# Performance work log

Measured on AMD Instinct MI355X. Metric: run time of the kernel, lower is better.

## Reference

```python
import jax, jax.numpy as jnp
import numpy as np


def setup_inputs() -> dict:
    key = jax.random.key(0)
    k1, k2, k3, k4 = jax.random.split(key, 4)
    b, l, v, s = 2, 2048, 8, 64
    return {
        "query": jax.random.normal(k1, (b, l, v, s), dtype=jnp.float32),
        "key": jax.random.normal(k2, (b, l, v, s), dtype=jnp.float32),
        "value": jax.random.normal(k3, (b, l, v, s), dtype=jnp.float32),
        "label_arr": jax.random.randint(k4, (b, l), 0, 8, dtype=jnp.int64),
    }


def reference(query, key, value, label_arr):
    # query/key/value: (b, l, v, s); label_arr computed into a mask in the
    # original code but never applied, so it does not affect the math.
    b, l, v, s = query.shape
    scale = 1.0 / np.sqrt(s).astype(np.float32)
    # key summed over the v (head) axis -> pooled key per token: (b, l, s)
    sum_tot_vec = key.sum(axis=2)
    # scores[b,l,v,m] = <query[b,l,v,:], sum_tot_vec[b,m,:]>  (the torch per-v loop, batched)
    scores = jnp.einsum("blvs,bms->blvm", query, sum_tot_vec)
    A = jax.nn.softmax(scale * scores, axis=-1)  # (b, l, v, l)
    # V[b,l,v,s] = sum_m A[b,l,v,m] * value[b,m,v,s]  (the broadcast-multiply+sum, as a matmul)
    V = jnp.einsum("blvm,bmvs->blvs", A, value)
    return V
```

## Files before the change

kernel.cpp:

```cpp
#include <hip/hip_runtime.h>


#define BB 2
#define LL 2048
#define HH 8
#define DD 64

typedef __attribute__((ext_vector_type(8)))  short  short8;
typedef __attribute__((ext_vector_type(16))) float  float16v;

static __device__ inline unsigned short f2bf(float x) {
    union { float f; unsigned u; } v; v.f = x;
    unsigned r = v.u + 0x7FFF + ((v.u >> 16) & 1);
    return (unsigned short)(r >> 16);
}
static __device__ inline unsigned pk_bf2(float x, float y) {
    return (unsigned)f2bf(x) | ((unsigned)f2bf(y) << 16);
}

__global__ void pool_kernel(const float* __restrict__ key,
                            unsigned short* __restrict__ kswz) {
    int c  = blockIdx.x * blockDim.x + threadIdx.x;
    int r  = c >> 3;
    int ck = c & 7;
    int ks = ck >> 1, hf = ck & 1;
    int b = r >> 11, ml = r & 2047;
    int T = ml >> 5, ln = ml & 31;

    const float* base = key + ((size_t)r * HH) * DD + ks * 16 + hf * 8;
    float s[8];
#pragma unroll
    for (int j = 0; j < 8; ++j) s[j] = 0.f;
#pragma unroll
    for (int v = 0; v < HH; ++v) {
        float4 f0 = *(const float4*)(base + v * DD);
        float4 f1 = *(const float4*)(base + v * DD + 4);
        s[0] += f0.x; s[1] += f0.y; s[2] += f0.z; s[3] += f0.w;
        s[4] += f1.x; s[5] += f1.y; s[6] += f1.z; s[7] += f1.w;
    }
    union { short8 v; unsigned u[4]; } o;
#pragma unroll
    for (int i = 0; i < 4; ++i) o.u[i] = pk_bf2(s[2 * i], s[2 * i + 1]);
    *(short8*)(kswz + ((((size_t)b * 64 + T) * 4 + ks) * 512)
                    + (hf * 32 + ln) * 8) = o.v;
}

__global__ void vswz_kernel(const float* __restrict__ value,
                            unsigned short* __restrict__ vswz, int bh0) {
    int blk = blockIdx.x;
    int mt  = blk & 31;
    int bhl = blk >> 5;
    int bh  = bh0 + bhl;
    int h = bh & 7, b = bh >> 3;
    int m0 = mt * 64;
    int tid = threadIdx.x;

    __shared__ __align__(16) float Vl[64][68];

#pragma unroll
    for (int k = 0; k < 4; ++k) {
        int f = tid + k * 256;
        int r = f >> 4;
        int cc = (f & 15) * 4;
        float4 t = *(const float4*)(value +
            (((size_t)(b * LL + m0 + r)) * HH + h) * DD + cc);
        *(float4*)&Vl[r][cc] = t;
    }
    __syncthreads();

#pragma unroll
    for (int k = 0; k < 2; ++k) {
        int c    = tid + k * 256;
        int Tl   = c >> 8;
        int t    = (c >> 7) & 1;
        int vh   = (c >> 6) & 1;
        int lane = c & 63;
        int ln = lane & 31, half = lane >> 5;
        union { short8 v; unsigned short u[8]; } o;
#pragma unroll
        for (int jj = 0; jj < 8; ++jj) {
            int r2  = t * 8 + jj;
            int key = (r2 & 3) + 8 * (r2 >> 2) + 4 * half;
            o.u[jj] = f2bf(Vl[Tl * 32 + key][vh * 32 + ln]);
        }
        *(short8*)(vswz + ((((size_t)bhl * 64 + (mt * 2 + Tl)) * 4 + t * 2 + vh) * 512)
                        + lane * 8) = o.v;
    }
}

__global__ __launch_bounds__(512, 4)
void attn_kernel(const float* __restrict__ query,
                 const unsigned short* __restrict__ kswz,
                 const unsigned short* __restrict__ vswz,
                 float* __restrict__ out, int bh0) {
    constexpr int NIT = 8;

    int bid = blockIdx.x;
    int qt  = bid & 63;
    int bhl = bid >> 6;
    int bh  = bh0 + bhl;
    int h = bh & 7, b = bh >> 3;

    int tid  = threadIdx.x;
    int lane = tid & 63;
    int wv   = tid >> 6;
    int ln   = lane & 31;
    int half = lane >> 5;

    __shared__ float O4[4][32][DD];
    __shared__ float lsumL[4][64];
    __shared__ float invL[32];

    short8 qf[4];
    const float* qbase = query + (((size_t)(b * LL + qt * 32 + ln)) * HH + h) * DD;
#pragma unroll
    for (int ks = 0; ks < 4; ++ks) {
        const float4* qp = (const float4*)(qbase + ks * 16 + half * 8);
        float4 t0 = qp[0], t1 = qp[1];
        union { short8 v; unsigned u[4]; } uq;
        uq.u[0] = pk_bf2(t0.x * 0.125f, t0.y * 0.125f);
        uq.u[1] = pk_bf2(t0.z * 0.125f, t0.w * 0.125f);
        uq.u[2] = pk_bf2(t1.x * 0.125f, t1.y * 0.125f);
        uq.u[3] = pk_bf2(t1.z * 0.125f, t1.w * 0.125f);
        qf[ks] = uq.v;
    }

    const unsigned short* kp0 = kswz + (((size_t)b * 64 + wv * 8) * 4) * 512
                                     + (size_t)lane * 8;
    const unsigned short* vp0 = vswz + (((size_t)bhl * 64 + wv * 8) * 4) * 512
                                     + (size_t)lane * 8;

    float16v o0, o1;
#pragma unroll
    for (int i = 0; i < 16; ++i) { o0[i] = 0.f; o1[i] = 0.f; }
    float lsum = 0.f;

    short8 kf[4];
#pragma unroll
    for (int ks = 0; ks < 4; ++ks) kf[ks] = *(const short8*)(kp0 + ks * 512);

#pragma unroll
    for (int it = 0; it < NIT; ++it) {
        short8 vf[4];
#pragma unroll
        for (int u = 0; u < 4; ++u)
            vf[u] = *(const short8*)(vp0 + it * 2048 + u * 512);

        float16v sacc;
#pragma unroll
        for (int i = 0; i < 16; ++i) sacc[i] = 0.f;
#pragma unroll
        for (int ks = 0; ks < 4; ++ks)
            sacc = __builtin_amdgcn_mfma_f32_32x32x16_bf16(kf[ks], qf[ks], sacc, 0, 0, 0);

        short8 kn[4];
        if (it + 1 < NIT) {
#pragma unroll
            for (int ks = 0; ks < 4; ++ks)
                kn[ks] = *(const short8*)(kp0 + (it + 1) * 2048 + ks * 512);
        }

        union { short8 v[2]; unsigned u[8]; } pu;
#pragma unroll
        for (int i = 0; i < 8; ++i) {
            union { float f; unsigned u; } e0, e1;
            e0.f = __expf(sacc[2 * i]);
            e1.f = __expf(sacc[2 * i + 1]);
            lsum += e0.f + e1.f;
            pu.u[i] = __builtin_amdgcn_perm(e1.u + 0x8000u, e0.u + 0x8000u, 0x07060302u);
        }

#pragma unroll
        for (int t = 0; t < 2; ++t) {
            o0 = __builtin_amdgcn_mfma_f32_32x32x16_bf16(pu.v[t], vf[t * 2 + 0], o0, 0, 0, 0);
            o1 = __builtin_amdgcn_mfma_f32_32x32x16_bf16(pu.v[t], vf[t * 2 + 1], o1, 0, 0, 0);
        }

        if (it + 1 < NIT) {
#pragma unroll
            for (int ks = 0; ks < 4; ++ks) kf[ks] = kn[ks];
        }
    }

    if (wv < 4) {
        lsumL[wv][lane] = lsum;
#pragma unroll
        for (int r = 0; r < 16; ++r) {
            int row = (r & 3) + 8 * (r >> 2) + 4 * half;
            O4[wv][row][ln]      = o0[r];
            O4[wv][row][32 + ln] = o1[r];
        }
    }
    __syncthreads();
    if (wv >= 4) {
        lsumL[wv - 4][lane] += lsum;
#pragma unroll
        for (int r = 0; r < 16; ++r) {
            int row = (r & 3) + 8 * (r >> 2) + 4 * half;
            O4[wv - 4][row][ln]      += o0[r];
            O4[wv - 4][row][32 + ln] += o1[r];
        }
    }
    __syncthreads();

    if (tid < 32) {
        float s = 0.f;
#pragma unroll
        for (int w = 0; w < 4; ++w) s += lsumL[w][tid] + lsumL[w][tid + 32];
        invL[tid] = 1.0f / s;
    }
    __syncthreads();

    int qrow = tid >> 4;
    int c4   = (tid & 15) * 4;
    float inv = invL[qrow];
    float4 r;
    r.x = (O4[0][qrow][c4 + 0] + O4[1][qrow][c4 + 0] + O4[2][qrow][c4 + 0] + O4[3][qrow][c4 + 0]) * inv;
    r.y = (O4[0][qrow][c4 + 1] + O4[1][qrow][c4 + 1] + O4[2][qrow][c4 + 1] + O4[3][qrow][c4 + 1]) * inv;
    r.z = (O4[0][qrow][c4 + 2] + O4[1][qrow][c4 + 2] + O4[2][qrow][c4 + 2] + O4[3][qrow][c4 + 2]) * inv;
    r.w = (O4[0][qrow][c4 + 3] + O4[1][qrow][c4 + 3] + O4[2][qrow][c4 + 3] + O4[3][qrow][c4 + 3]) * inv;
    *(float4*)(out + (((size_t)(b * LL + qt * 32 + qrow)) * HH + h) * DD + c4) = r;
}

extern "C" void kernel_launch(void* const* d_in, const int* in_sizes, int n_in,
                              void* d_out, int out_size, void* d_ws, size_t ws_size,
                              hipStream_t stream) {
    const float* query = (const float*)d_in[0];
    const float* key   = (const float*)d_in[1];
    const float* value = (const float*)d_in[2];
    float* out = (float*)d_out;

    unsigned short* kswz = (unsigned short*)d_ws;
    unsigned short* vswz = (unsigned short*)((char*)d_ws + 512 * 1024);

    size_t avail = (ws_size > (size_t)(512 * 1024)) ? ws_size - 512 * 1024 : 0;
    int nbh = (int)(avail / ((size_t)DD * LL * 2));
    if (nbh >= 16) nbh = 16; else if (nbh >= 8) nbh = 8;
    else if (nbh >= 4) nbh = 4; else if (nbh >= 2) nbh = 2; else nbh = 1;

    pool_kernel<<<(BB * LL * 8) / 256, 256, 0, stream>>>(key, kswz);

    for (int bh0 = 0; bh0 < BB * HH; bh0 += nbh) {
        vswz_kernel<<<nbh * 32, 256, 0, stream>>>(value, vswz, bh0);
        attn_kernel<<<nbh * 64, 512, 0, stream>>>(query, kswz, vswz, out, bh0);
    }
}
```

Before: 105.4 us.

## Fuse prep kernels, process 64 queries per block, use exp2 with pre-scaled keys

Merges the key pooling and value swizzle into one prep kernel and drops the workspace-size-dependent per-head loop, so only two launches remain. The attention block now covers 64 query rows with 4 waves instead of 32 rows with 8 waves, so each K/V fragment load is reused for two query groups. It also folds log2(e) into the pooled keys so the softmax can use exp2f. The trade-off is fewer blocks (512 of 256 threads) and more registers per wave, and the code now assumes the workspace can hold all 16 heads of swizzled V at once.

Result: no change. 107.2 us (+1.8%).

```diff
diff --git a/kernel.cpp b/kernel.cpp
--- a/kernel.cpp
+++ b/kernel.cpp
@@ -18,87 +18,82 @@
     return (unsigned)f2bf(x) | ((unsigned)f2bf(y) << 16);
 }
 
-__global__ void pool_kernel(const float* __restrict__ key,
-                            unsigned short* __restrict__ kswz) {
-    int c  = blockIdx.x * blockDim.x + threadIdx.x;
-    int r  = c >> 3;
-    int ck = c & 7;
-    int ks = ck >> 1, hf = ck & 1;
-    int b = r >> 11, ml = r & 2047;
-    int T = ml >> 5, ln = ml & 31;
-
-    const float* base = key + ((size_t)r * HH) * DD + ks * 16 + hf * 8;
-    float s[8];
-#pragma unroll
-    for (int j = 0; j < 8; ++j) s[j] = 0.f;
-#pragma unroll
-    for (int v = 0; v < HH; ++v) {
-        float4 f0 = *(const float4*)(base + v * DD);
-        float4 f1 = *(const float4*)(base + v * DD + 4);
-        s[0] += f0.x; s[1] += f0.y; s[2] += f0.z; s[3] += f0.w;
-        s[4] += f1.x; s[5] += f1.y; s[6] += f1.z; s[7] += f1.w;
-    }
-    union { short8 v; unsigned u[4]; } o;
-#pragma unroll
-    for (int i = 0; i < 4; ++i) o.u[i] = pk_bf2(s[2 * i], s[2 * i + 1]);
-    *(short8*)(kswz + ((((size_t)b * 64 + T) * 4 + ks) * 512)
-                    + (hf * 32 + ln) * 8) = o.v;
-}
-
-__global__ void vswz_kernel(const float* __restrict__ value,
-                            unsigned short* __restrict__ vswz, int bh0) {
-    int blk = blockIdx.x;
-    int mt  = blk & 31;
-    int bhl = blk >> 5;
-    int bh  = bh0 + bhl;
-    int h = bh & 7, b = bh >> 3;
-    int m0 = mt * 64;
+__global__ __launch_bounds__(256)
+void prep_kernel(const float* __restrict__ key, const float* __restrict__ value,
+                 unsigned short* __restrict__ kswz,
+                 unsigned short* __restrict__ vswz) {
+    __shared__ __align__(16) float Vl[64][68];
+    int bid = blockIdx.x;
     int tid = threadIdx.x;
 
-    __shared__ __align__(16) float Vl[64][68];
-
-#pragma unroll
-    for (int k = 0; k < 4; ++k) {
-        int f = tid + k * 256;
-        int r = f >> 4;
-        int cc = (f & 15) * 4;
-        float4 t = *(const float4*)(value +
-            (((size_t)(b * LL + m0 + r)) * HH + h) * DD + cc);
-        *(float4*)&Vl[r][cc] = t;
-    }
-    __syncthreads();
-
-#pragma unroll
-    for (int k = 0; k < 2; ++k) {
-        int c    = tid + k * 256;
-        int Tl   = c >> 8;
-        int t    = (c >> 7) & 1;
-        int vh   = (c >> 6) & 1;
-        int lane = c & 63;
-        int ln = lane & 31, half = lane >> 5;
-        union { short8 v; unsigned short u[8]; } o;
-#pragma unroll
-        for (int jj = 0; jj < 8; ++jj) {
-            int r2  = t * 8 + jj;
-            int key = (r2 & 3) + 8 * (r2 >> 2) + 4 * half;
-            o.u[jj] = f2bf(Vl[Tl * 32 + key][vh * 32 + ln]);
-        }
-        *(short8*)(vswz + ((((size_t)bhl * 64 + (mt * 2 + Tl)) * 4 + t * 2 + vh) * 512)
-                        + lane * 8) = o.v;
-    }
-}
-
-__global__ __launch_bounds__(512, 4)
+    if (bid < 512) {
+        int mt = bid & 31, bh = bid >> 5;
+        int h = bh & 7, b = bh >> 3;
+        int m0 = mt * 64;
+#pragma unroll
+        for (int k = 0; k < 4; ++k) {
+            int f = tid + k * 256;
+            int r = f >> 4;
+            int cc = (f & 15) * 4;
+            float4 t = *(const float4*)(value +
+                (((size_t)(b * LL + m0 + r)) * HH + h) * DD + cc);
+            *(float4*)&Vl[r][cc] = t;
+        }
+        __syncthreads();
+#pragma unroll
+        for (int k = 0; k < 2; ++k) {
+            int c    = tid + k * 256;
+            int Tl   = c >> 8;
+            int t    = (c >> 7) & 1;
+            int vh   = (c >> 6) & 1;
+            int lane = c & 63;
+            int ln = lane & 31, half = lane >> 5;
+            union { short8 v; unsigned short u[8]; } o;
+#pragma unroll
+            for (int jj = 0; jj < 8; ++jj) {
+                int r2 = t * 8 + jj;
+                int m  = (r2 & 3) + 8 * (r2 >> 2) + 4 * half;
+                o.u[jj] = f2bf(Vl[Tl * 32 + m][vh * 32 + ln]);
+            }
+            *(short8*)(vswz +
+                ((((size_t)bh * 64 + (mt * 2 + Tl)) * 4 + t * 2 + vh) * 512)
+                + lane * 8) = o.v;
+        }
+    } else {
+        const float LOG2E = 1.4426950408889634f;
+        int pb    = bid - 512;
+        int chunk = pb * 4 + (tid >> 6);
+        int lane  = tid & 63;
+        int b = chunk >> 8, T = (chunk >> 2) & 63, ks = chunk & 3;
+        int ln = lane & 31, hf = lane >> 5;
+        const float* base = key + (((size_t)(b * LL + T * 32 + ln)) * HH) * DD
+                                + ks * 16 + hf * 8;
+        float s[8];
+#pragma unroll
+        for (int j = 0; j < 8; ++j) s[j] = 0.f;
+#pragma unroll
+        for (int v = 0; v < HH; ++v) {
+            float4 f0 = *(const float4*)(base + v * DD);
+            float4 f1 = *(const float4*)(base + v * DD + 4);
+            s[0] += f0.x; s[1] += f0.y; s[2] += f0.z; s[3] += f0.w;
+            s[4] += f1.x; s[5] += f1.y; s[6] += f1.z; s[7] += f1.w;
+        }
+        union { short8 v; unsigned u[4]; } o;
+#pragma unroll
+        for (int i = 0; i < 4; ++i)
+            o.u[i] = pk_bf2(s[2 * i] * LOG2E, s[2 * i + 1] * LOG2E);
+        *(short8*)(kswz + (size_t)chunk * 512 + lane * 8) = o.v;
+    }
+}
+
+__global__ __launch_bounds__(256, 3)
 void attn_kernel(const float* __restrict__ query,
                  const unsigned short* __restrict__ kswz,
                  const unsigned short* __restrict__ vswz,
-                 float* __restrict__ out, int bh0) {
-    constexpr int NIT = 8;
-
+                 float* __restrict__ out) {
     int bid = blockIdx.x;
-    int qt  = bid & 63;
-    int bhl = bid >> 6;
-    int bh  = bh0 + bhl;
+    int bh  = bid & 15;
+    int qt  = bid >> 4;
     int h = bh & 7, b = bh >> 3;
 
     int tid  = threadIdx.x;
@@ -107,119 +102,129 @@
     int ln   = lane & 31;
     int half = lane >> 5;
 
-    __shared__ float O4[4][32][DD];
-    __shared__ float lsumL[4][64];
-    __shared__ float invL[32];
-
-    short8 qf[4];
-    const float* qbase = query + (((size_t)(b * LL + qt * 32 + ln)) * HH + h) * DD;
-#pragma unroll
-    for (int ks = 0; ks < 4; ++ks) {
-        const float4* qp = (const float4*)(qbase + ks * 16 + half * 8);
-        float4 t0 = qp[0], t1 = qp[1];
-        union { short8 v; unsigned u[4]; } uq;
-        uq.u[0] = pk_bf2(t0.x * 0.125f, t0.y * 0.125f);
-        uq.u[1] = pk_bf2(t0.z * 0.125f, t0.w * 0.125f);
-        uq.u[2] = pk_bf2(t1.x * 0.125f, t1.y * 0.125f);
-        uq.u[3] = pk_bf2(t1.z * 0.125f, t1.w * 0.125f);
-        qf[ks] = uq.v;
-    }
-
-    const unsigned short* kp0 = kswz + (((size_t)b * 64 + wv * 8) * 4) * 512
+    __shared__ float O2[2][64][68];
+    __shared__ float lsumL[4][128];
+    __shared__ float invL[64];
+
+    short8 qf[2][4];
+#pragma unroll
+    for (int g = 0; g < 2; ++g) {
+        const float* qbase = query +
+            (((size_t)(b * LL + qt * 64 + g * 32 + ln)) * HH + h) * DD;
+#pragma unroll
+        for (int ks = 0; ks < 4; ++ks) {
+            const float4* qp = (const float4*)(qbase + ks * 16 + half * 8);
+            float4 t0 = qp[0], t1 = qp[1];
+            union { short8 v; unsigned u[4]; } uq;
+            uq.u[0] = pk_bf2(t0.x * 0.125f, t0.y * 0.125f);
+            uq.u[1] = pk_bf2(t0.z * 0.125f, t0.w * 0.125f);
+            uq.u[2] = pk_bf2(t1.x * 0.125f, t1.y * 0.125f);
+            uq.u[3] = pk_bf2(t1.z * 0.125f, t1.w * 0.125f);
+            qf[g][ks] = uq.v;
+        }
+    }
+
+    const unsigned short* kp0 = kswz + (((size_t)b * 64 + wv * 16) * 4) * 512
                                      + (size_t)lane * 8;
-    const unsigned short* vp0 = vswz + (((size_t)bhl * 64 + wv * 8) * 4) * 512
+    const unsigned short* vp0 = vswz + (((size_t)bh * 64 + wv * 16) * 4) * 512
                                      + (size_t)lane * 8;
 
-    float16v o0, o1;
-#pragma unroll
-    for (int i = 0; i < 16; ++i) { o0[i] = 0.f; o1[i] = 0.f; }
-    float lsum = 0.f;
-
-    short8 kf[4];
-#pragma unroll
-    for (int ks = 0; ks < 4; ++ks) kf[ks] = *(const short8*)(kp0 + ks * 512);
-
-#pragma unroll
-    for (int it = 0; it < NIT; ++it) {
-        short8 vf[4];
+    float16v o00, o01, o10, o11;
+#pragma unroll
+    for (int i = 0; i < 16; ++i) { o00[i] = 0.f; o01[i] = 0.f; o10[i] = 0.f; o11[i] = 0.f; }
+    float ls0a = 0.f, ls0b = 0.f, ls1a = 0.f, ls1b = 0.f;
+
+#pragma unroll
+    for (int it = 0; it < 16; ++it) {
+        short8 kf[4], vf[4];
+#pragma unroll
+        for (int ks = 0; ks < 4; ++ks)
+            kf[ks] = *(const short8*)(kp0 + it * 2048 + ks * 512);
 #pragma unroll
         for (int u = 0; u < 4; ++u)
             vf[u] = *(const short8*)(vp0 + it * 2048 + u * 512);
 
-        float16v sacc;
-#pragma unroll
-        for (int i = 0; i < 16; ++i) sacc[i] = 0.f;
-#pragma unroll
-        for (int ks = 0; ks < 4; ++ks)
-            sacc = __builtin_amdgcn_mfma_f32_32x32x16_bf16(kf[ks], qf[ks], sacc, 0, 0, 0);
-
-        short8 kn[4];
-        if (it + 1 < NIT) {
+#pragma unroll
+        for (int g = 0; g < 2; ++g) {
+            float16v sacc;
+#pragma unroll
+            for (int i = 0; i < 16; ++i) sacc[i] = 0.f;
 #pragma unroll
             for (int ks = 0; ks < 4; ++ks)
-                kn[ks] = *(const short8*)(kp0 + (it + 1) * 2048 + ks * 512);
-        }
-
-        union { short8 v[2]; unsigned u[8]; } pu;
-#pragma unroll
-        for (int i = 0; i < 8; ++i) {
-            union { float f; unsigned u; } e0, e1;
-            e0.f = __expf(sacc[2 * i]);
-            e1.f = __expf(sacc[2 * i + 1]);
-            lsum += e0.f + e1.f;
-            pu.u[i] = __builtin_amdgcn_perm(e1.u + 0x8000u, e0.u + 0x8000u, 0x07060302u);
-        }
-
-#pragma unroll
-        for (int t = 0; t < 2; ++t) {
-            o0 = __builtin_amdgcn_mfma_f32_32x32x16_bf16(pu.v[t], vf[t * 2 + 0], o0, 0, 0, 0);
-            o1 = __builtin_amdgcn_mfma_f32_32x32x16_bf16(pu.v[t], vf[t * 2 + 1], o1, 0, 0, 0);
-        }
-
-        if (it + 1 < NIT) {
-#pragma unroll
-            for (int ks = 0; ks < 4; ++ks) kf[ks] = kn[ks];
-        }
-    }
-
-    if (wv < 4) {
-        lsumL[wv][lane] = lsum;
+                sacc = __builtin_amdgcn_mfma_f32_32x32x16_bf16(kf[ks], qf[g][ks], sacc, 0, 0, 0);
+
+            union { short8 v[2]; unsigned u[8]; } pu;
+#pragma unroll
+            for (int i = 0; i < 8; ++i) {
+                union { float f; unsigned u; } e0, e1;
+                e0.f = exp2f(sacc[2 * i]);
+                e1.f = exp2f(sacc[2 * i + 1]);
+                if (g == 0) { ls0a += e0.f; ls0b += e1.f; }
+                else        { ls1a += e0.f; ls1b += e1.f; }
+                pu.u[i] = __builtin_amdgcn_perm(e1.u + 0x8000u, e0.u + 0x8000u, 0x07060302u);
+            }
+
+            if (g == 0) {
+                o00 = __builtin_amdgcn_mfma_f32_32x32x16_bf16(pu.v[0], vf[0], o00, 0, 0, 0);
+                o01 = __builtin_amdgcn_mfma_f32_32x32x16_bf16(pu.v[0], vf[1], o01, 0, 0, 0);
+                o00 = __builtin_amdgcn_mfma_f32_32x32x16_bf16(pu.v[1], vf[2], o00, 0, 0, 0);
+                o01 = __builtin_amdgcn_mfma_f32_32x32x16_bf16(pu.v[1], vf[3], o01, 0, 0, 0);
+            } else {
+                o10 = __builtin_amdgcn_mfma_f32_32x32x16_bf16(pu.v[0], vf[0], o10, 0, 0, 0);
+                o11 = __builtin_amdgcn_mfma_f32_32x32x16_bf16(pu.v[0], vf[1], o11, 0, 0, 0);
+                o10 = __builtin_amdgcn_mfma_f32_32x32x16_bf16(pu.v[1], vf[2], o10, 0, 0, 0);
+                o11 = __builtin_amdgcn_mfma_f32_32x32x16_bf16(pu.v[1], vf[3], o11, 0, 0, 0);
+            }
+        }
+    }
+
+    lsumL[wv][lane]      = ls0a + ls0b;
+    lsumL[wv][64 + lane] = ls1a + ls1b;
+    if (wv < 2) {
 #pragma unroll
         for (int r = 0; r < 16; ++r) {
             int row = (r & 3) + 8 * (r >> 2) + 4 * half;
-            O4[wv][row][ln]      = o0[r];
-            O4[wv][row][32 + ln] = o1[r];
+            O2[wv][row][ln]           = o00[r];
+            O2[wv][row][32 + ln]      = o01[r];
+            O2[wv][32 + row][ln]      = o10[r];
+            O2[wv][32 + row][32 + ln] = o11[r];
         }
     }
     __syncthreads();
-    if (wv >= 4) {
-        lsumL[wv - 4][lane] += lsum;
+    if (wv >= 2) {
 #pragma unroll
         for (int r = 0; r < 16; ++r) {
             int row = (r & 3) + 8 * (r >> 2) + 4 * half;
-            O4[wv - 4][row][ln]      += o0[r];
-            O4[wv - 4][row][32 + ln] += o1[r];
+            O2[wv - 2][row][ln]           += o00[r];
+            O2[wv - 2][row][32 + ln]      += o01[r];
+            O2[wv - 2][32 + row][ln]      += o10[r];
+            O2[wv - 2][32 + row][32 + ln] += o11[r];
         }
     }
     __syncthreads();
 
-    if (tid < 32) {
+    if (tid < 64) {
+        int g = tid >> 5, c = tid & 31;
         float s = 0.f;
 #pragma unroll
-        for (int w = 0; w < 4; ++w) s += lsumL[w][tid] + lsumL[w][tid + 32];
+        for (int w = 0; w < 4; ++w)
+            s += lsumL[w][g * 64 + c] + lsumL[w][g * 64 + 32 + c];
         invL[tid] = 1.0f / s;
     }
     __syncthreads();
 
-    int qrow = tid >> 4;
-    int c4   = (tid & 15) * 4;
+    int qrow = tid >> 2;
+    int c16  = (tid & 3) * 16;
     float inv = invL[qrow];
-    float4 r;
-    r.x = (O4[0][qrow][c4 + 0] + O4[1][qrow][c4 + 0] + O4[2][qrow][c4 + 0] + O4[3][qrow][c4 + 0]) * inv;
-    r.y = (O4[0][qrow][c4 + 1] + O4[1][qrow][c4 + 1] + O4[2][qrow][c4 + 1] + O4[3][qrow][c4 + 1]) * inv;
-    r.z = (O4[0][qrow][c4 + 2] + O4[1][qrow][c4 + 2] + O4[2][qrow][c4 + 2] + O4[3][qrow][c4 + 2]) * inv;
-    r.w = (O4[0][qrow][c4 + 3] + O4[1][qrow][c4 + 3] + O4[2][qrow][c4 + 3] + O4[3][qrow][c4 + 3]) * inv;
-    *(float4*)(out + (((size_t)(b * LL + qt * 32 + qrow)) * HH + h) * DD + c4) = r;
+    float buf[16];
+#pragma unroll
+    for (int j = 0; j < 16; ++j)
+        buf[j] = (O2[0][qrow][c16 + j] + O2[1][qrow][c16 + j]) * inv;
+    float* ob = out + (((size_t)(b * LL + qt * 64 + qrow)) * HH + h) * DD + c16;
+#pragma unroll
+    for (int j = 0; j < 4; ++j)
+        *(float4*)(ob + 4 * j) = make_float4(buf[4 * j], buf[4 * j + 1],
+                                             buf[4 * j + 2], buf[4 * j + 3]);
 }
 
 extern "C" void kernel_launch(void* const* d_in, const int* in_sizes, int n_in,
@@ -233,15 +238,6 @@
     unsigned short* kswz = (unsigned short*)d_ws;
     unsigned short* vswz = (unsigned short*)((char*)d_ws + 512 * 1024);
 
-    size_t avail = (ws_size > (size_t)(512 * 1024)) ? ws_size - 512 * 1024 : 0;
-    int nbh = (int)(avail / ((size_t)DD * LL * 2));
-    if (nbh >= 16) nbh = 16; else if (nbh >= 8) nbh = 8;
-    else if (nbh >= 4) nbh = 4; else if (nbh >= 2) nbh = 2; else nbh = 1;
-
-    pool_kernel<<<(BB * LL * 8) / 256, 256, 0, stream>>>(key, kswz);
-
-    for (int bh0 = 0; bh0 < BB * HH; bh0 += nbh) {
-        vswz_kernel<<<nbh * 32, 256, 0, stream>>>(value, vswz, bh0);
-        attn_kernel<<<nbh * 64, 512, 0, stream>>>(query, kswz, vswz, out, bh0);
-    }
-}
+    prep_kernel<<<640, 256, 0, stream>>>(key, value, kswz, vswz);
+    attn_kernel<<<512, 256, 0, stream>>>(query, kswz, vswz, out);
+}
```
